# Kernel tuning notes

Hardware: AMD Instinct MI355X
Metric: run time of the kernel (lower is better)

Reference implementation:

```python
import jax, jax.numpy as jnp
import numpy as np

HIDDEN = 1024
HEADS = 16
HEAD = HIDDEN // HEADS
EXPAND = 4096
EPS = 1e-5


def layer_norm(x, g, b):
    mu = jnp.mean(x, axis=-1, keepdims=True)
    var = jnp.mean((x - mu) ** 2, axis=-1, keepdims=True)
    return (x - mu) * jax.lax.rsqrt(var + EPS) * g + b


def setup_inputs() -> dict:
    key = jax.random.key(0)
    ks = jax.random.split(key, 12)
    s = 0.02
    return {
        "x": jax.random.normal(ks[0], (4, 2048, HIDDEN), dtype=jnp.float32),
        "Wqkv": jax.random.normal(ks[1], (HIDDEN, 3 * HIDDEN), dtype=jnp.float32) * s,
        "bqkv": jnp.zeros((3 * HIDDEN,), jnp.float32),
        "Wproj": jax.random.normal(ks[2], (HIDDEN, HIDDEN), dtype=jnp.float32) * s,
        "bproj": jnp.zeros((HIDDEN,), jnp.float32),
        "W1": jax.random.normal(ks[3], (HIDDEN, EXPAND), dtype=jnp.float32) * s,
        "b1": jnp.zeros((EXPAND,), jnp.float32),
        "W2": jax.random.normal(ks[4], (EXPAND, HIDDEN), dtype=jnp.float32) * s,
        "b2": jnp.zeros((HIDDEN,), jnp.float32),
        "g1": jnp.ones((HIDDEN,), jnp.float32),
        "be1": jnp.zeros((HIDDEN,), jnp.float32),
        "g2": jnp.ones((HIDDEN,), jnp.float32),
        "be2": jnp.zeros((HIDDEN,), jnp.float32),
    }


def attention(x, Wqkv, bqkv, Wproj, bproj):
    B, L, _ = x.shape
    qkv = (x @ Wqkv + bqkv).reshape(B, L, 3, HEADS, HEAD)
    q, k, v = [qkv[:, :, i].transpose(0, 2, 1, 3) for i in range(3)]  # [B,H,L,D]
    attn = jnp.einsum("bnld,bnkd->bnlk", q, k) / np.sqrt(HEAD).astype(np.float32)
    attn = jax.nn.softmax(attn, axis=-1)
    o = jnp.einsum("bnlk,bnkd->bnld", attn, v)
    o = o.transpose(0, 2, 1, 3).reshape(B, L, HIDDEN)
    return o @ Wproj + bproj


def reference(x, Wqkv, bqkv, Wproj, bproj, W1, b1, W2, b2, g1, be1, g2, be2):
    # post-norm transformer block (pre_norm=False), dropout=0 (eval)
    h = layer_norm(x + attention(x, Wqkv, bqkv, Wproj, bproj), g1, be1)
    ff = jax.nn.gelu(h @ W1 + b1, approximate=False) @ W2 + b2
    return layer_norm(h + ff, g2, be2)
```

## Files before the change

### kernel.cpp

```cpp
#include <hip/hip_runtime.h>
#include <hip/hip_bf16.h>
#include <math.h>


typedef __bf16 bf16_t;
typedef __bf16 bf16x8 __attribute__((ext_vector_type(8)));
typedef __bf16 bf16x4 __attribute__((ext_vector_type(4)));
typedef float f32x4 __attribute__((ext_vector_type(4)));
typedef float f32x16 __attribute__((ext_vector_type(16)));

#define HID   1024
#define NHEAD 16
#define HD    64
#define EXPD  4096
#define LSEQ  2048
#define BATCH 4
#define MROWS (BATCH * LSEQ)

#if __has_builtin(__builtin_amdgcn_exp2f)
#define EXP2F __builtin_amdgcn_exp2f
#else
#define EXP2F exp2f
#endif

__device__ __forceinline__ void gld_lds16(const bf16_t* g, bf16_t* l) {
  __builtin_amdgcn_global_load_lds(
      (const __attribute__((address_space(1))) void*)g,
      (__attribute__((address_space(3))) void*)l, 16, 0, 0);
}

__device__ __forceinline__ void vmwait(int n) {
  if (n == 4)      asm volatile("s_waitcnt vmcnt(4)" ::: "memory");
  else if (n == 3) asm volatile("s_waitcnt vmcnt(3)" ::: "memory");
  else if (n == 0) asm volatile("s_waitcnt vmcnt(0)" ::: "memory");
}

__device__ __forceinline__ void block_bar() {
  asm volatile("" ::: "memory");
  __builtin_amdgcn_s_barrier();
  asm volatile("" ::: "memory");
}

__device__ __forceinline__ void swap32(unsigned& a, unsigned& b) {
#if __has_builtin(__builtin_amdgcn_permlane32_swap)
  auto r = __builtin_amdgcn_permlane32_swap(a, b, false, false);
  a = r[0]; b = r[1];
#else
  bool hiL = ((threadIdx.x & 63) >= 32);
  unsigned pa = (unsigned)__shfl_xor((int)a, 32, 64);
  unsigned pb = (unsigned)__shfl_xor((int)b, 32, 64);
  unsigned na = hiL ? pb : a;
  unsigned nb = hiL ? b : pa;
  a = na; b = nb;
#endif
}

__device__ __forceinline__ unsigned pk_bf16(float lo, float hi) {
  bf16_t l = (bf16_t)lo, h = (bf16_t)hi;
  unsigned short ul, uh;
  __builtin_memcpy(&ul, &l, 2);
  __builtin_memcpy(&uh, &h, 2);
  return (unsigned)ul | ((unsigned)uh << 16);
}

__global__ __launch_bounds__(256) void cvt_bf16(const float* __restrict__ in,
                                                bf16_t* __restrict__ out, int n4) {
  int i = blockIdx.x * 256 + threadIdx.x;
  if (i >= n4) return;
  float4 v = ((const float4*)in)[i];
  bf16x4 o;
  o[0] = (bf16_t)v.x; o[1] = (bf16_t)v.y; o[2] = (bf16_t)v.z; o[3] = (bf16_t)v.w;
  ((bf16x4*)out)[i] = o;
}

__global__ __launch_bounds__(256) void transpose_cvt(const float* __restrict__ W,
                                                     bf16_t* __restrict__ Wt,
                                                     int K, int N) {
  __shared__ float tile[32][33];
  int n0 = blockIdx.x * 32, k0 = blockIdx.y * 32;
  int tx = threadIdx.x & 31, ty = threadIdx.x >> 5;
#pragma unroll
  for (int i = 0; i < 32; i += 8)
    tile[ty + i][tx] = W[(size_t)(k0 + ty + i) * N + n0 + tx];
  __syncthreads();
#pragma unroll
  for (int i = 0; i < 32; i += 8)
    Wt[(size_t)(n0 + ty + i) * K + k0 + tx] = (bf16_t)tile[tx][ty + i];
}

__global__ __launch_bounds__(256) void transpose_v(const bf16_t* __restrict__ qkvb,
                                                   bf16_t* __restrict__ vT) {
  __shared__ bf16_t tile[64][65];
  const int l0 = blockIdx.x * 64;
  const int bh = blockIdx.y;
  const int b = bh >> 4, h = bh & 15;
  const int tx = threadIdx.x & 63, ty = threadIdx.x >> 6;
  const bf16_t* src = qkvb + ((size_t)(b * LSEQ + l0)) * 3072 + 2048 + h * 64;
#pragma unroll
  for (int i = 0; i < 16; ++i) {
    int l = ty + 4 * i;
    tile[l][tx] = src[(size_t)l * 3072 + tx];
  }
  __syncthreads();
  bf16_t* dst = vT + ((size_t)bh * HD) * LSEQ + l0;
#pragma unroll
  for (int i = 0; i < 16; ++i) {
    int d = ty + 4 * i;
    dst[(size_t)d * LSEQ + tx] = tile[tx][d];
  }
}

template <int BM, int BN, int NTHR>
__global__ __launch_bounds__(NTHR, (NTHR == 512 ? 4 : 3))
void gemm_k(const bf16_t* __restrict__ A,
            const bf16_t* __restrict__ Bt,
            const float* __restrict__ bias,
            void* __restrict__ C,
            int M, int N, int K, int mode) {
  constexpr int WC = (NTHR / 64) / 2;
  constexpr int AL = BM * 4 / NTHR;
  constexpr int BL = BN * 4 / NTHR;
  constexpr int LOADS = AL + BL;
  constexpr int RSTEP = NTHR >> 2;
  __shared__ bf16_t As[3 * BM * 32];
  __shared__ bf16_t Bs[3 * BN * 32];

  const int nbx = gridDim.x;
  int p = blockIdx.y * nbx + blockIdx.x;
  const int GM = 8;
  int group = p / (GM * nbx);
  int idx = p - group * (GM * nbx);
  const int by = group * GM + (idx & (GM - 1));
  const int bx = idx >> 3;
  const int n0 = bx * BN, m0 = by * BM;

  const int t = threadIdx.x;
  const int lane = t & 63, w = t >> 6;
  const int wr = w / WC, wc = w % WC;
  const int quad = lane >> 4, l16 = lane & 15;

  f32x4 acc[4][4];
#pragma unroll
  for (int i = 0; i < 4; ++i)
#pragma unroll
    for (int j = 0; j < 4; ++j) acc[i][j] = (f32x4){0.f, 0.f, 0.f, 0.f};

  const int r0 = t >> 2;
  const unsigned ksw = (((unsigned)t & 3u) ^ ((unsigned)(r0 >> 1) & 3u)) * 8u;
  const unsigned offR0 = (unsigned)r0 * (unsigned)K + ksw;

  const bf16_t* aB = A + (size_t)m0 * K;
  const bf16_t* bB = Bt + (size_t)n0 * K;

  unsigned aoff[4], boff[4];
#pragma unroll
  for (int i = 0; i < 4; ++i) {
    int row = wr * 64 + 16 * i + l16;
    aoff[i] = (unsigned)(row * 32 + (quad ^ ((row >> 1) & 3)) * 8);
  }
#pragma unroll
  for (int j = 0; j < 4; ++j) {
    int row = wc * 64 + 16 * j + l16;
    boff[j] = (unsigned)(row * 32 + (quad ^ ((row >> 1) & 3)) * 8);
  }

  auto stage = [&](int slot, int kk) {
    bf16_t* Asl = As + slot * (BM * 32);
    bf16_t* Bsl = Bs + slot * (BN * 32);
    const bf16_t* aS = aB + kk;
    const bf16_t* bS = bB + kk;
#pragma unroll
    for (int a = 0; a < AL; ++a)
      gld_lds16(aS + offR0 + (size_t)a * RSTEP * K, Asl + (t + a * NTHR) * 8);
#pragma unroll
    for (int b = 0; b < BL; ++b)
      gld_lds16(bS + offR0 + (size_t)b * RSTEP * K, Bsl + (t + b * NTHR) * 8);
  };

  const int NT = K >> 5;

  stage(0, 0);
  stage(1, 32);
  vmwait(LOADS);
  block_bar();

  int cs = 0;
  for (int kt = 0; kt < NT; ++kt) {
    if (kt < NT - 2) {
      int ss = cs == 0 ? 2 : cs - 1;
      stage(ss, (kt + 2) * 32);
    }
    const bf16_t* Asl = As + cs * (BM * 32);
    const bf16_t* Bsl = Bs + cs * (BN * 32);
    bf16x8 af[4], bfr[4];
#pragma unroll
    for (int i = 0; i < 4; ++i) af[i] = *(const bf16x8*)(Asl + aoff[i]);
#pragma unroll
    for (int j = 0; j < 4; ++j) bfr[j] = *(const bf16x8*)(Bsl + boff[j]);
    __builtin_amdgcn_s_setprio(1);
#pragma unroll
    for (int i = 0; i < 4; ++i)
#pragma unroll
      for (int j = 0; j < 4; ++j)
        acc[i][j] = __builtin_amdgcn_mfma_f32_16x16x32_bf16(af[i], bfr[j], acc[i][j], 0, 0, 0);
    __builtin_amdgcn_s_setprio(0);
    if (kt < NT - 2)      vmwait(LOADS);
    else if (kt == NT - 2) vmwait(0);
    if (kt < NT - 1) block_bar();
    cs = cs == 2 ? 0 : cs + 1;
  }

#pragma unroll
  for (int i = 0; i < 4; ++i) {
    int rowb = m0 + wr * 64 + 16 * i + quad * 4;
#pragma unroll
    for (int j = 0; j < 4; ++j) {
      int col = n0 + wc * 64 + 16 * j + l16;
      float bv = bias[col];
#pragma unroll
      for (int r = 0; r < 4; ++r) {
        float v = acc[i][j][r] + bv;
        size_t idx = (size_t)(rowb + r) * N + col;
        if (mode == 0) {
          ((bf16_t*)C)[idx] = (bf16_t)v;
        } else if (mode == 1) {
          float u = v * (0.7978845608028654f + 0.0356774081f * v * v);
          float e = EXP2F(u * 2.885390082f);
          float th = (e - 1.f) / (e + 1.f);
          float gel = 0.5f * v * (1.f + th);
          ((bf16_t*)C)[idx] = (bf16_t)gel;
        } else {
          ((float*)C)[idx] = v;
        }
      }
    }
  }
}

__global__ __launch_bounds__(256) void attn_kernel(const bf16_t* __restrict__ qkv,
                                                   const bf16_t* __restrict__ vT,
                                                   bf16_t* __restrict__ ob) {
  __shared__ bf16_t smem[3 * 128 * 64];
  bf16_t* Ks  = smem;
  bf16_t* Vts = smem + 8192;
  bf16_t* Qs  = smem + 16384;
  const int qt = blockIdx.x, h = blockIdx.y, b = blockIdx.z;
  const int t = threadIdx.x, lane = t & 63, w = t >> 6;
  const int l32 = lane & 31, hi = lane >> 5;
  const size_t RS = 3 * HID;
  const int bh = b * NHEAD + h;

  const bf16_t* qbase = qkv + ((size_t)(b * LSEQ + qt * 128)) * RS + h * HD;
  const bf16_t* kbase = qkv + ((size_t)b * LSEQ) * RS + HID + h * HD;
  const bf16_t* vtbase = vT + (size_t)bh * HD * LSEQ;

#pragma unroll
  for (int s = 0; s < 4; ++s) {
    int l = t + s * 256;
    int r = l >> 3, c8 = l & 7;
    gld_lds16(qbase + (size_t)r * RS + ((c8 ^ (r & 7)) * 8), Qs + l * 8);
  }
  __syncthreads();

  const float sc = 0.18033688011112042f;
  bf16x8 bq[4];
  {
    int qrow = 32 * w + l32;
#pragma unroll
    for (int c = 0; c < 4; ++c) {
      int y = 2 * c + hi;
      bf16x8 q8 = *(const bf16x8*)(Qs + qrow * 64 + ((y ^ (qrow & 7)) * 8));
#pragma unroll
      for (int e = 0; e < 8; ++e) q8[e] = (bf16_t)((float)q8[e] * sc);
      bq[c] = q8;
    }
  }

  f32x16 accO[2];
#pragma unroll
  for (int dt = 0; dt < 2; ++dt)
#pragma unroll
    for (int e = 0; e < 16; ++e) accO[dt][e] = 0.f;
  float l_acc = 0.f;

  for (int kt = 0; kt < LSEQ / 128; ++kt) {
    __syncthreads();
#pragma unroll
    for (int s = 0; s < 4; ++s) {
      int l = t + s * 256;
      int r = l >> 3, c8 = l & 7;
      gld_lds16(kbase + (size_t)(kt * 128 + r) * RS + ((c8 ^ (r & 7)) * 8), Ks + l * 8);
      int rv = l >> 4, c16 = l & 15;
      gld_lds16(vtbase + (size_t)rv * LSEQ + kt * 128 + ((c16 ^ (rv & 7)) * 8), Vts + l * 8);
    }
    __syncthreads();

#pragma unroll
    for (int kt2 = 0; kt2 < 2; ++kt2) {
      f32x16 s0, s1;
#pragma unroll
      for (int e = 0; e < 16; ++e) { s0[e] = 0.f; s1[e] = 0.f; }
#pragma unroll
      for (int c = 0; c < 4; ++c) {
        int y = 2 * c + hi;
        int r0 = (2 * kt2 + 0) * 32 + l32;
        bf16x8 a0 = *(const bf16x8*)(Ks + r0 * 64 + ((y ^ (r0 & 7)) * 8));
        s0 = __builtin_amdgcn_mfma_f32_32x32x16_bf16(a0, bq[c], s0, 0, 0, 0);
        int r1 = (2 * kt2 + 1) * 32 + l32;
        bf16x8 a1 = *(const bf16x8*)(Ks + r1 * 64 + ((y ^ (r1 & 7)) * 8));
        s1 = __builtin_amdgcn_mfma_f32_32x32x16_bf16(a1, bq[c], s1, 0, 0, 0);
      }

      unsigned pf[2][2][4];
#pragma unroll
      for (int tile = 0; tile < 2; ++tile) {
        f32x16& sv = tile ? s1 : s0;
        float p[16];
#pragma unroll
        for (int e = 0; e < 16; ++e) { p[e] = EXP2F(sv[e]); l_acc += p[e]; }
        unsigned lo[4], hi_[4];
#pragma unroll
        for (int g = 0; g < 4; ++g) {
          lo[g] = pk_bf16(p[4 * g + 0], p[4 * g + 1]);
          hi_[g] = pk_bf16(p[4 * g + 2], p[4 * g + 3]);
        }
#pragma unroll
        for (int c2 = 0; c2 < 2; ++c2) {
          unsigned aL = lo[2 * c2], bL = lo[2 * c2 + 1];
          swap32(aL, bL);
          pf[tile][c2][0] = aL; pf[tile][c2][2] = bL;
          unsigned aH = hi_[2 * c2], bH = hi_[2 * c2 + 1];
          swap32(aH, bH);
          pf[tile][c2][1] = aH; pf[tile][c2][3] = bH;
        }
      }

#pragma unroll
      for (int dt = 0; dt < 2; ++dt)
#pragma unroll
        for (int tile = 0; tile < 2; ++tile)
#pragma unroll
          for (int c2 = 0; c2 < 2; ++c2) {
            int ktile = 2 * kt2 + tile;
            int c8v = ktile * 4 + c2 * 2 + hi;
            int rv = dt * 32 + l32;
            bf16x8 av = *(const bf16x8*)(Vts + rv * 128 + ((c8v ^ (rv & 7)) * 8));
            union { unsigned u[4]; bf16x8 v; } bp;
            bp.u[0] = pf[tile][c2][0]; bp.u[1] = pf[tile][c2][1];
            bp.u[2] = pf[tile][c2][2]; bp.u[3] = pf[tile][c2][3];
            accO[dt] = __builtin_amdgcn_mfma_f32_32x32x16_bf16(av, bp.v, accO[dt], 0, 0, 0);
          }
    }
  }

  l_acc += __shfl_xor(l_acc, 32, 64);
  float inv = 1.f / l_acc;

  __syncthreads();
  bf16_t* Osh = smem;
  {
    int q = 32 * w + l32;
#pragma unroll
    for (int dt = 0; dt < 2; ++dt)
#pragma unroll
      for (int e = 0; e < 16; ++e) {
        int d = dt * 32 + (e & 3) + 8 * (e >> 2) + 4 * hi;
        Osh[q * 68 + d] = (bf16_t)(accO[dt][e] * inv);
      }
  }
  __syncthreads();
#pragma unroll
  for (int s = 0; s < 4; ++s) {
    int l = t + s * 256;
    int r = l >> 3, c8 = l & 7;
    bf16x8 v = *(const bf16x8*)(Osh + r * 68 + c8 * 8);
    *(bf16x8*)(ob + ((size_t)(b * LSEQ + qt * 128 + r)) * HID + h * HD + c8 * 8) = v;
  }
}

__global__ __launch_bounds__(256) void resid_ln(const float* __restrict__ X,
                                                const float* __restrict__ Y,
                                                const float* __restrict__ g,
                                                const float* __restrict__ be,
                                                float* __restrict__ outf,
                                                bf16_t* __restrict__ outb) {
  const int row = blockIdx.x;
  const int t = threadIdx.x;
  float4 a = ((const float4*)X)[(size_t)row * 256 + t];
  float4 bvec = ((const float4*)Y)[(size_t)row * 256 + t];
  float v0 = a.x + bvec.x, v1 = a.y + bvec.y, v2 = a.z + bvec.z, v3 = a.w + bvec.w;
  float s = v0 + v1 + v2 + v3;
  float s2 = v0 * v0 + v1 * v1 + v2 * v2 + v3 * v3;
#pragma unroll
  for (int msk = 1; msk < 64; msk <<= 1) {
    s += __shfl_xor(s, msk, 64);
    s2 += __shfl_xor(s2, msk, 64);
  }
  __shared__ float red[8];
  int w = t >> 6;
  if ((t & 63) == 0) { red[w] = s; red[w + 4] = s2; }
  __syncthreads();
  s = red[0] + red[1] + red[2] + red[3];
  s2 = red[4] + red[5] + red[6] + red[7];
  float mu = s * (1.f / 1024.f);
  float var = s2 * (1.f / 1024.f) - mu * mu;
  float rstd = rsqrtf(var + 1e-5f);
  float4 gg = ((const float4*)g)[t];
  float4 bb = ((const float4*)be)[t];
  float o0 = (v0 - mu) * rstd * gg.x + bb.x;
  float o1 = (v1 - mu) * rstd * gg.y + bb.y;
  float o2 = (v2 - mu) * rstd * gg.z + bb.z;
  float o3 = (v3 - mu) * rstd * gg.w + bb.w;
  float4 o = {o0, o1, o2, o3};
  ((float4*)outf)[(size_t)row * 256 + t] = o;
  if (outb) {
    bf16x4 ob4;
    ob4[0] = (bf16_t)o0; ob4[1] = (bf16_t)o1; ob4[2] = (bf16_t)o2; ob4[3] = (bf16_t)o3;
    ((bf16x4*)outb)[(size_t)row * 256 + t] = ob4;
  }
}

extern "C" void kernel_launch(void* const* d_in, const int* in_sizes, int n_in,
                              void* d_out, int out_size, void* d_ws, size_t ws_size,
                              hipStream_t stream) {
  const float* x     = (const float*)d_in[0];
  const float* Wqkv  = (const float*)d_in[1];
  const float* bqkv  = (const float*)d_in[2];
  const float* Wproj = (const float*)d_in[3];
  const float* bproj = (const float*)d_in[4];
  const float* W1    = (const float*)d_in[5];
  const float* b1    = (const float*)d_in[6];
  const float* W2    = (const float*)d_in[7];
  const float* b2    = (const float*)d_in[8];
  const float* g1    = (const float*)d_in[9];
  const float* be1   = (const float*)d_in[10];
  const float* g2    = (const float*)d_in[11];
  const float* be2   = (const float*)d_in[12];
  float* out = (float*)d_out;

  char* ws = (char*)d_ws;
  size_t off = 0;
  auto alloc = [&](size_t bytes) -> char* {
    char* p = ws + off;
    off += (bytes + 255) & ~(size_t)255;
    return p;
  };
  bf16_t* wqkvT  = (bf16_t*)alloc((size_t)3072 * 1024 * 2);
  bf16_t* wprojT = (bf16_t*)alloc((size_t)1024 * 1024 * 2);
  bf16_t* w1T    = (bf16_t*)alloc((size_t)4096 * 1024 * 2);
  bf16_t* w2T    = (bf16_t*)alloc((size_t)1024 * 4096 * 2);
  char*   xb_ob  = alloc((size_t)MROWS * HID * 2);
  char*   qkv_ff = alloc((size_t)MROWS * EXPD * 2);
  char*   a_f2   = alloc((size_t)MROWS * HID * 4);
  float*  h      = (float*)alloc((size_t)MROWS * HID * 4);
  bf16_t* hb     = (bf16_t*)alloc((size_t)MROWS * HID * 2);

  bf16_t* xb    = (bf16_t*)xb_ob;
  bf16_t* ob    = (bf16_t*)xb_ob;
  bf16_t* qkvb  = (bf16_t*)qkv_ff;
  bf16_t* ff1b  = (bf16_t*)qkv_ff;
  float*  attnf = (float*)a_f2;
  float*  ff2f  = (float*)a_f2;
  bf16_t* vTg   = hb;

  dim3 blk(256);
  dim3 blk512(512);
  transpose_cvt<<<dim3(3072 / 32, 1024 / 32), blk, 0, stream>>>(Wqkv, wqkvT, 1024, 3072);
  transpose_cvt<<<dim3(1024 / 32, 1024 / 32), blk, 0, stream>>>(Wproj, wprojT, 1024, 1024);
  transpose_cvt<<<dim3(4096 / 32, 1024 / 32), blk, 0, stream>>>(W1, w1T, 1024, 4096);
  transpose_cvt<<<dim3(1024 / 32, 4096 / 32), blk, 0, stream>>>(W2, w2T, 4096, 1024);
  cvt_bf16<<<MROWS * HID / 4 / 256, blk, 0, stream>>>(x, xb, MROWS * HID / 4);

  gemm_k<128, 256, 512><<<dim3(3072 / 256, MROWS / 128), blk512, 0, stream>>>(
      xb, wqkvT, bqkv, qkvb, MROWS, 3072, 1024, 0);
  transpose_v<<<dim3(LSEQ / 64, BATCH * NHEAD), blk, 0, stream>>>(qkvb, vTg);
  attn_kernel<<<dim3(LSEQ / 128, NHEAD, BATCH), blk, 0, stream>>>(qkvb, vTg, ob);
  gemm_k<128, 128, 256><<<dim3(1024 / 128, MROWS / 128), blk, 0, stream>>>(
      ob, wprojT, bproj, attnf, MROWS, 1024, 1024, 2);
  resid_ln<<<MROWS, blk, 0, stream>>>(x, attnf, g1, be1, h, hb);
  gemm_k<128, 256, 512><<<dim3(4096 / 256, MROWS / 128), blk512, 0, stream>>>(
      hb, w1T, b1, ff1b, MROWS, 4096, 1024, 1);
  gemm_k<128, 128, 256><<<dim3(1024 / 128, MROWS / 128), blk, 0, stream>>>(
      ff1b, w2T, b2, ff2f, MROWS, 1024, 4096, 2);
  resid_ln<<<MROWS, blk, 0, stream>>>(h, ff2f, g2, be2, out, (bf16_t*)nullptr);
}
```

Measured before the change: 571.7 us.

## Double-buffer K/V tiles in attention with async prefetch and MFMA priority

Attention now uses two LDS slots for K/V tiles. The next tile is issued through global_load_lds before the current one is computed, and a partial vmcnt wait lets the loads overlap the MFMA work. s_setprio is raised around the MFMA sections, and launch bounds request 2 blocks per CU. LDS use grows to 80KB per block, which may cap occupancy, and the per-iteration barrier pattern changes.

```diff
diff --git a/kernel.cpp b/kernel.cpp
--- a/kernel.cpp
+++ b/kernel.cpp
@@ -30,7 +30,8 @@
 }
 
 __device__ __forceinline__ void vmwait(int n) {
-  if (n == 4)      asm volatile("s_waitcnt vmcnt(4)" ::: "memory");
+  if (n == 8)      asm volatile("s_waitcnt vmcnt(8)" ::: "memory");
+  else if (n == 4) asm volatile("s_waitcnt vmcnt(4)" ::: "memory");
   else if (n == 3) asm volatile("s_waitcnt vmcnt(3)" ::: "memory");
   else if (n == 0) asm volatile("s_waitcnt vmcnt(0)" ::: "memory");
 }
@@ -237,13 +238,11 @@
   }
 }
 
-__global__ __launch_bounds__(256) void attn_kernel(const bf16_t* __restrict__ qkv,
-                                                   const bf16_t* __restrict__ vT,
-                                                   bf16_t* __restrict__ ob) {
-  __shared__ bf16_t smem[3 * 128 * 64];
-  bf16_t* Ks  = smem;
-  bf16_t* Vts = smem + 8192;
-  bf16_t* Qs  = smem + 16384;
+__global__ __launch_bounds__(256, 2) void attn_kernel(const bf16_t* __restrict__ qkv,
+                                                      const bf16_t* __restrict__ vT,
+                                                      bf16_t* __restrict__ ob) {
+  __shared__ bf16_t smem[5 * 128 * 64];
+  bf16_t* Qs = smem + 32768;
   const int qt = blockIdx.x, h = blockIdx.y, b = blockIdx.z;
   const int t = threadIdx.x, lane = t & 63, w = t >> 6;
   const int l32 = lane & 31, hi = lane >> 5;
@@ -276,15 +275,9 @@
     }
   }
 
-  f32x16 accO[2];
-#pragma unroll
-  for (int dt = 0; dt < 2; ++dt)
-#pragma unroll
-    for (int e = 0; e < 16; ++e) accO[dt][e] = 0.f;
-  float l_acc = 0.f;
-
-  for (int kt = 0; kt < LSEQ / 128; ++kt) {
-    __syncthreads();
+  auto stageKV = [&](int slot, int kt) {
+    bf16_t* Ks = smem + slot * 16384;
+    bf16_t* Vts = Ks + 8192;
 #pragma unroll
     for (int s = 0; s < 4; ++s) {
       int l = t + s * 256;
@@ -293,13 +286,36 @@
       int rv = l >> 4, c16 = l & 15;
       gld_lds16(vtbase + (size_t)rv * LSEQ + kt * 128 + ((c16 ^ (rv & 7)) * 8), Vts + l * 8);
     }
-    __syncthreads();
+  };
+
+  f32x16 accO[2];
+#pragma unroll
+  for (int dt = 0; dt < 2; ++dt)
+#pragma unroll
+    for (int e = 0; e < 16; ++e) accO[dt][e] = 0.f;
+  float l_acc = 0.f;
+
+  constexpr int NT = LSEQ / 128;
+  stageKV(0, 0);
+
+  for (int kt = 0; kt < NT; ++kt) {
+    const int cs = kt & 1;
+    if (kt + 1 < NT) {
+      stageKV(1 - cs, kt + 1);
+      vmwait(8);
+    } else {
+      vmwait(0);
+    }
+    block_bar();
+    const bf16_t* Ks = smem + cs * 16384;
+    const bf16_t* Vts = Ks + 8192;
 
 #pragma unroll
     for (int kt2 = 0; kt2 < 2; ++kt2) {
       f32x16 s0, s1;
 #pragma unroll
       for (int e = 0; e < 16; ++e) { s0[e] = 0.f; s1[e] = 0.f; }
+      __builtin_amdgcn_s_setprio(1);
 #pragma unroll
       for (int c = 0; c < 4; ++c) {
         int y = 2 * c + hi;
@@ -310,6 +326,7 @@
         bf16x8 a1 = *(const bf16x8*)(Ks + r1 * 64 + ((y ^ (r1 & 7)) * 8));
         s1 = __builtin_amdgcn_mfma_f32_32x32x16_bf16(a1, bq[c], s1, 0, 0, 0);
       }
+      __builtin_amdgcn_s_setprio(0);
 
       unsigned pf[2][2][4];
 #pragma unroll
@@ -335,6 +352,7 @@
         }
       }
 
+      __builtin_amdgcn_s_setprio(1);
 #pragma unroll
       for (int dt = 0; dt < 2; ++dt)
 #pragma unroll
@@ -350,13 +368,14 @@
             bp.u[2] = pf[tile][c2][2]; bp.u[3] = pf[tile][c2][3];
             accO[dt] = __builtin_amdgcn_mfma_f32_32x32x16_bf16(av, bp.v, accO[dt], 0, 0, 0);
           }
+      __builtin_amdgcn_s_setprio(0);
     }
+    block_bar();
   }
 
   l_acc += __shfl_xor(l_acc, 32, 64);
   float inv = 1.f / l_acc;
 
-  __syncthreads();
   bf16_t* Osh = smem;
   {
     int q = 32 * w + l32;
```

After: 569.1 us. Within noise of the previous version (-0.5%).
